# Optimization experiments

Measured on AMD Instinct MI355X. Metric: run time of the kernel, lower is better.

The kernel has to match this reference:

```python
import jax, jax.numpy as jnp
import numpy as np

H = 256          # encoder hidden per direction
D = 2 * H        # decoder hidden / bidirectional feature dim
IN = 2
OUT = 2
B = 64
T = 256
STEPS = 24       # hard-coded decoder loop length in the source


def gru_cell(x, h, Wih, Whh, bih, bhh):
    # PyTorch GRU cell: gate order (r, z, n)
    gi = x @ Wih.T + bih
    gh = h @ Whh.T + bhh
    ir, iz, inn = jnp.split(gi, 3, axis=-1)
    hr, hz, hn = jnp.split(gh, 3, axis=-1)
    r = jax.nn.sigmoid(ir + hr)
    z = jax.nn.sigmoid(iz + hz)
    n = jnp.tanh(inn + r * hn)
    return (1.0 - z) * n + z * h


def run_dir(xs, Wih, Whh, bih, bhh, reverse):
    # xs: (T, B, F) time-major; returns outputs (T, B, H) and last hidden (B, H)
    h0 = jnp.zeros((xs.shape[1], Whh.shape[-1]), xs.dtype)
    def step(h, xt):
        h2 = gru_cell(xt, h, Wih, Whh, bih, bhh)
        return h2, h2
    h_last, ys = jax.lax.scan(step, h0, xs, reverse=reverse)
    return ys, h_last


def setup_inputs():
    keys = jax.random.split(jax.random.key(0), 24)
    k = iter(keys)
    def rn(shape, s):
        return jax.random.normal(next(k), shape, jnp.float32) * s
    se = 1.0 / np.sqrt(H)
    sd = 1.0 / np.sqrt(D)
    return {
        "x": rn((B, T, IN), 1.0),
        "enc_Wih0": rn((2, 3 * H, IN), se),
        "enc_Whh0": rn((2, 3 * H, H), se),
        "enc_bih0": rn((2, 3 * H), se),
        "enc_bhh0": rn((2, 3 * H), se),
        "enc_Wih": rn((2, 2, 3 * H, D), se),
        "enc_Whh": rn((2, 2, 3 * H, H), se),
        "enc_bih": rn((2, 2, 3 * H), se),
        "enc_bhh": rn((2, 2, 3 * H), se),
        "dec_Wih": rn((3, 3 * D, D), sd),
        "dec_Whh": rn((3, 3 * D, D), sd),
        "dec_bih": rn((3, 3 * D), sd),
        "dec_bhh": rn((3, 3 * D), sd),
        "fc_con_W": rn((D, 2 * D), sd),
        "fc_con_b": rn((D,), sd),
        "attn_W": rn((D, 2 * D), sd),
        "attn_b": rn((D,), sd),
        "v": jax.random.uniform(next(k), (D,), jnp.float32),  # torch.rand init
        "fc_W": rn((OUT, D), sd),
        "fc_b": rn((OUT,), sd),
    }


def reference(x, enc_Wih0, enc_Whh0, enc_bih0, enc_bhh0,
              enc_Wih, enc_Whh, enc_bih, enc_bhh,
              dec_Wih, dec_Whh, dec_bih, dec_bhh,
              fc_con_W, fc_con_b, attn_W, attn_b, v, fc_W, fc_b):
    # ---- bidirectional 3-layer GRU encoder ----
    seq = x.transpose(1, 0, 2)  # (T, B, IN) time-major
    hf_list, hb_list = [], []
    for l in range(3):
        if l == 0:
            Wf, Uf, bf, cf = enc_Wih0[0], enc_Whh0[0], enc_bih0[0], enc_bhh0[0]
            Wb, Ub, bb, cb = enc_Wih0[1], enc_Whh0[1], enc_bih0[1], enc_bhh0[1]
        else:
            Wf, Uf, bf, cf = enc_Wih[l-1, 0], enc_Whh[l-1, 0], enc_bih[l-1, 0], enc_bhh[l-1, 0]
            Wb, Ub, bb, cb = enc_Wih[l-1, 1], enc_Whh[l-1, 1], enc_bih[l-1, 1], enc_bhh[l-1, 1]
        yf, hf = run_dir(seq, Wf, Uf, bf, cf, False)
        yb, hb = run_dir(seq, Wb, Ub, bb, cb, True)
        seq = jnp.concatenate([yf, yb], axis=-1)
        hf_list.append(hf)
        hb_list.append(hb)
    enc_out = seq.transpose(1, 0, 2)  # (B, T, D)
    # hidden_decoder = cat(forward, backward) per layer -> (3, B, D)
    hidden = jnp.stack([jnp.concatenate([f, b], axis=-1)
                        for f, b in zip(hf_list, hb_list)])
    dec_in = enc_out[:, -1, :]  # (B, D)

    # additive attention: energy = tanh(W [h; enc_out] + b); precompute enc part
    attn_Wh = attn_W[:, :D]
    attn_We = attn_W[:, D:]
    enc_proj = jnp.einsum('bte,de->btd', enc_out, attn_We)  # (B, T, D)

    def dec_step(carry, _):
        d_in, hid = carry
        hq = hid[-1] @ attn_Wh.T                               # (B, D)
        energy = jnp.tanh(hq[:, None, :] + enc_proj + attn_b)  # (B, T, D)
        scores = jnp.einsum('btd,d->bt', energy, v)
        aw = jax.nn.softmax(scores, axis=1)                    # (B, T)
        ctx = jnp.einsum('bt,btd->bd', aw, enc_out)            # (B, D)
        inp = jnp.concatenate([d_in, ctx], axis=-1) @ fc_con_W.T + fc_con_b
        new_h = []
        for l in range(3):  # 3-layer unidirectional decoder GRU, single step
            hl = gru_cell(inp, hid[l], dec_Wih[l], dec_Whh[l], dec_bih[l], dec_bhh[l])
            new_h.append(hl)
            inp = hl
        out_step = inp @ fc_W.T + fc_b
        return (inp, jnp.stack(new_h)), out_step

    _, outs = jax.lax.scan(dec_step, (dec_in, hidden), None, length=STEPS)
    return outs.transpose(1, 0, 2)  # (B, 24, OUT)
```

## Files before the change

### kernel.cpp

```cpp
#include <hip/hip_runtime.h>

typedef unsigned short u16;
typedef unsigned int u32;
typedef _Float16 f16;
typedef f16   f16x2 __attribute__((ext_vector_type(2)));
typedef f16   f16x8 __attribute__((ext_vector_type(8)));
typedef float f32x4 __attribute__((ext_vector_type(4)));

#define MFMA16(a,b,c) __builtin_amdgcn_mfma_f32_16x16x32_f16((a),(b),(c),0,0,0)

__device__ __forceinline__ float sigm_(float x){ return 1.f/(1.f + __expf(-x)); }
__device__ __forceinline__ float tanh_(float x){ return 1.f - 2.f/(1.f + __expf(2.f*x)); }
__device__ __forceinline__ float clampf(float x, float c){
  if (!(x > -c)) x = -c;
  if (x > c) x = c;
  return x;
}
__device__ __forceinline__ f16x8 cvt8f(const float* p){
  const float4 a = *(const float4*)p;
  const float4 b = *(const float4*)(p+4);
  f16x8 r;
  r[0]=(f16)a.x; r[1]=(f16)a.y; r[2]=(f16)a.z; r[3]=(f16)a.w;
  r[4]=(f16)b.x; r[5]=(f16)b.y; r[6]=(f16)b.z; r[7]=(f16)b.w;
  return r;
}

__global__ void k_diag(float* out, int mib){
  const int i = blockIdx.x*256 + threadIdx.x;
  if (i < 3072) out[i] = 1000.f * (float)mib;
}

__global__ void k_prep_dec(const float* dWhh, const float* attnW, const float* fccon,
                           const float* dWih, f16* R3)
{
  long idx = (long)blockIdx.x*256 + threadIdx.x;
  const float* src; int rs, colOff = 0, NKS; long dst, loc;
  if (idx < 294912L) {
    loc = idx; const int m = (int)(loc / 98304); loc %= 98304;
    src = dWhh + (long)m*786432; rs = 512; NKS = 16; dst = (long)m*786432;
  } else if (idx < 327680L) {
    loc = idx - 294912L; src = attnW; colOff = 512; rs = 1024; NKS = 16; dst = 2359296L;
  } else if (idx < 393216L) {
    loc = idx - 327680L; src = fccon; rs = 1024; NKS = 32; dst = 2621440L;
  } else if (idx < 688128L) {
    loc = idx - 393216L; const int m = (int)(loc / 98304); loc %= 98304;
    src = dWih + (long)m*786432; rs = 512; NKS = 16; dst = 3440640L + (long)m*786432;
  } else if (idx < 720896L) {
    loc = idx - 688128L; src = attnW; colOff = 0; rs = 1024; NKS = 16; dst = 5799936L;
  } else return;
  const int lane = (int)(loc & 63);
  const long frag = loc >> 6;
  const int ks = (int)(frag % NKS);
  const long nt = frag / NKS;
  const int n  = (int)(nt*16 + (lane & 15));
  const int k0 = ks*32 + ((lane >> 4) << 3);
  const float* sp = src + (long)n*rs + colOff + k0;
  f16* dp = R3 + dst + loc*8;
  #pragma unroll
  for (int j = 0; j < 8; ++j) dp[j] = (f16)sp[j];
}

__global__ void k_gi0s(const float* __restrict__ x, const float* __restrict__ W,
                       const float* __restrict__ bi, f16* __restrict__ gi,
                       int seg, int BH, int lbh, int b0)
{
  const long idx = (long)blockIdx.x*256 + threadIdx.x;
  const int v = (int)(idx % 24);
  long rest = idx / 24;
  const int tid = (int)(rest & 511); rest >>= 9;
  const int bq = (int)(rest & ((1 << (lbh-4)) - 1)); rest >>= (lbh-4);
  const int s = (int)(rest & 63);
  const int d = (int)(rest >> 6);
  const int r = v / 6, rem = v % 6, i = rem / 3, g = rem % 3;
  const int w = tid >> 6, q = (tid >> 4) & 3, lo = tid & 15;
  const int n = g*256 + (2*w + i)*16 + lo;
  const int b = bq*16 + q*4 + r;
  const int t = d ? (255 - (seg*64 + s)) : (seg*64 + s);
  const float x0 = x[(((b0+b)<<8) + t)*2];
  const float x1 = x[(((b0+b)<<8) + t)*2 + 1];
  const long wi = ((long)d*768 + n)*2;
  gi[idx] = (f16)clampf(x0*W[wi] + x1*W[wi+1] + bi[d*768 + n], 32.f);
}

#define GIE(G, vv) ((float)((vv) < 8 ? (G)[0][(vv)&7] : ((vv) < 16 ? (G)[1][(vv)-8] : (G)[2][(vv)-16])))

__global__ __launch_bounds__(512, 1) void k_enc_seg(
    const f16* __restrict__ gi, const float* __restrict__ Wraw,
    const float* __restrict__ bhh, f16* __restrict__ seq, int ostr,
    f16* __restrict__ fin, float* __restrict__ hcar, int seg, int BH)
{
  const int tid = threadIdx.x;
  const int w = tid >> 6, lane = tid & 63;
  const int lo16 = lane & 15, quad = lane >> 4;
  const int nbq = BH >> 4;
  const int dir = blockIdx.x / nbq, bq = blockIdx.x % nbq;

  __shared__ f16 h16[4][16][264];

  const float* mat = Wraw + (long)dir*196608;
  f16x8 wr[6][8];
  #pragma unroll
  for (int p = 0; p < 3; ++p)
    #pragma unroll
    for (int i = 0; i < 2; ++i) {
      const int n = (p*16 + 2*w + i)*16 + lo16;
      #pragma unroll
      for (int ks = 0; ks < 8; ++ks)
        wr[p*2+i][ks] = cvt8f(mat + (long)n*256 + ks*32 + quad*8);
    }
  float bh_[3][2];
  #pragma unroll
  for (int p = 0; p < 3; ++p)
    #pragma unroll
    for (int i = 0; i < 2; ++i)
      bh_[p][i] = bhh[dir*768 + p*256 + (2*w+i)*16 + lo16];

  float hreg[2][4];
  if (seg == 0) {
    #pragma unroll
    for (int i = 0; i < 2; ++i)
      #pragma unroll
      for (int r = 0; r < 4; ++r) {
        hreg[i][r] = 0.f;
        h16[0][quad*4 + r][(2*w+i)*16 + lo16] = (f16)0.f;
      }
  } else {
    #pragma unroll
    for (int i = 0; i < 2; ++i) {
      const int c = (2*w+i)*16 + lo16;
      #pragma unroll
      for (int r = 0; r < 4; ++r) {
        const float v = hcar[((dir*BH) + bq*16 + quad*4 + r)*256 + c];
        hreg[i][r] = v;
        h16[0][quad*4 + r][c] = (f16)v;
      }
    }
  }

  const long gstep = (long)nbq*512*24;
  const f16* gbase = gi + (((long)dir*64*nbq + bq)*512 + tid)*24;
  f16x8 g0[3], g1[3];
  { const f16x8* gp = (const f16x8*)gbase; g0[0]=gp[0]; g0[1]=gp[1]; g0[2]=gp[2]; }

  const int frow = tid >> 5;
  const int fcol = (tid & 31) * 8;

  for (int s = 0; s < 64; ++s) {
    __syncthreads();
    if (s >= 2) {
      const int so = s - 2;
      const int t2 = dir ? (255 - (seg*64 + so)) : (seg*64 + so);
      const f16x8 hv = *(const f16x8*)&h16[(so+1)&3][frow][fcol];
      *(f16x8*)&seq[((long)t2*ostr + bq*16 + frow)*512 + dir*256 + fcol] = hv;
    }
    f32x4 acc[6];
    #pragma unroll
    for (int q = 0; q < 6; ++q) acc[q] = (f32x4){0.f,0.f,0.f,0.f};
    #pragma unroll
    for (int ks = 0; ks < 8; ++ks) {
      const f16x8 a = *(const f16x8*)&h16[s&3][lo16][ks*32 + quad*8];
      #pragma unroll
      for (int q = 0; q < 6; ++q)
        acc[q] = MFMA16(a, wr[q][ks], acc[q]);
    }
    if (s < 63) {
      const f16x8* gp = (const f16x8*)(gbase + (long)(s+1)*gstep);
      g1[0]=gp[0]; g1[1]=gp[1]; g1[2]=gp[2];
    }
    #pragma unroll
    for (int i = 0; i < 2; ++i) {
      const int c = (2*w+i)*16 + lo16;
      #pragma unroll
      for (int r = 0; r < 4; ++r) {
        const int row = quad*4 + r;
        const int v = r*6 + i*3;
        const float gir = GIE(g0, v);
        const float giz = GIE(g0, v+1);
        const float gin = GIE(g0, v+2);
        const float rv = sigm_(gir + acc[i][r]   + bh_[0][i]);
        const float zv = sigm_(giz + acc[2+i][r] + bh_[1][i]);
        const float nv = tanh_(gin + rv*(acc[4+i][r] + bh_[2][i]));
        float hn = (1.f - zv)*nv + zv*hreg[i][r];
        hn = clampf(hn, 2.f);
        hreg[i][r] = hn;
        h16[(s+1)&3][row][c] = (f16)hn;
        if (seg == 3 && s == 63) fin[(bq*16 + row)*512 + dir*256 + c] = (f16)hn;
      }
    }
    g0[0]=g1[0]; g0[1]=g1[1]; g0[2]=g1[2];
  }
  __syncthreads();
  #pragma unroll
  for (int so = 62; so < 64; ++so) {
    const int t2 = dir ? (255 - (seg*64 + so)) : (seg*64 + so);
    const f16x8 hv = *(const f16x8*)&h16[(so+1)&3][frow][fcol];
    *(f16x8*)&seq[((long)t2*ostr + bq*16 + frow)*512 + dir*256 + fcol] = hv;
  }
  #pragma unroll
  for (int i = 0; i < 2; ++i) {
    const int c = (2*w+i)*16 + lo16;
    #pragma unroll
    for (int r = 0; r < 4; ++r)
      hcar[((dir*BH) + bq*16 + quad*4 + r)*256 + c] = hreg[i][r];
  }
}

__global__ void k_gemm(const f16* __restrict__ A, int K,
                       const f16* __restrict__ Bsw, const float* __restrict__ Braw,
                       long bzs, int ldb, int koff,
                       const float* __restrict__ bias, int biaszs,
                       void* __restrict__ Cv, long czs, int ldc, int mode,
                       int tb0, int tb1, int tdirsgn, int lbh, int abstr, float cv)
{
  const int tid = threadIdx.x, w = tid>>6, lane = tid&63;
  const int lo16 = lane&15, quad = lane>>4;
  const int m0 = blockIdx.x*64 + w*16;
  const int n0 = blockIdx.y*128;
  const int z  = blockIdx.z;
  const int tbase = z ? tb1 : tb0;
  const int tdir  = z ? -tdirsgn : tdirsgn;
  const int NKS = K >> 5;
  const int mrow = m0 + lo16;
  const long arow = (long)(tbase + tdir*(mrow >> lbh))*abstr + (mrow & ((1<<lbh)-1));
  const f16* Ap = A + arow*K + quad*8;
  f32x4 acc[8];
  #pragma unroll
  for (int i=0;i<8;++i) acc[i]=(f32x4){0.f,0.f,0.f,0.f};
  if (Bsw) {
    const f16* Bp = Bsw + (long)z*bzs;
    for (int ks = 0; ks < NKS; ++ks) {
      const f16x8 a = *(const f16x8*)(Ap + ks*32);
      #pragma unroll
      for (int nt = 0; nt < 8; ++nt) {
        const f16x8 b = *(const f16x8*)(Bp + (((long)((n0>>4)+nt)*NKS + ks) << 9) + lane*8);
        acc[nt] = MFMA16(a, b, acc[nt]);
      }
    }
  } else {
    const float* Bp = Braw + (long)z*bzs;
    for (int ks = 0; ks < NKS; ++ks) {
      const f16x8 a = *(const f16x8*)(Ap + ks*32);
      #pragma unroll
      for (int nt = 0; nt < 8; ++nt) {
        const f16x8 b = cvt8f(Bp + (long)(n0 + nt*16 + lo16)*ldb + koff + ks*32 + quad*8);
        acc[nt] = MFMA16(a, b, acc[nt]);
      }
    }
  }
  #pragma unroll
  for (int nt = 0; nt < 8; ++nt) {
    const int n = n0 + nt*16 + lo16;
    const float bv = bias ? bias[z*biaszs + n] : 0.f;
    #pragma unroll
    for (int r = 0; r < 4; ++r) {
      const int m = m0 + quad*4 + r;
      const float val = clampf(acc[nt][r] + bv, cv);
      if (mode == 2) {
        const int s_ = m >> lbh, b_ = m & ((1<<lbh)-1);
        const int bq_ = b_ >> 4, q_ = (b_ >> 2) & 3, r_ = b_ & 3;
        const int g_ = n >> 8, j_ = (n >> 4) & 15, lo_ = n & 15;
        const long idx = ((((long)z*64 + s_)*(1<<(lbh-4)) + bq_)*512
                          + ((j_>>1)*64 + q_*16 + lo_))*24 + r_*6 + (j_&1)*3 + g_;
        ((f16*)Cv)[idx] = (f16)val;
      } else if (mode == 1)
        ((f16*)Cv)[(long)z*czs + (long)m*ldc + n] = (f16)val;
      else
        ((float*)Cv)[(long)z*czs + (long)m*ldc + n] = val;
    }
  }
}

__global__ void k_score(const f16* __restrict__ seq, const f16* __restrict__ We,
                        const float* __restrict__ hq, const float* __restrict__ ab,
                        const float* __restrict__ vp, float* __restrict__ S)
{
  const int t = blockIdx.x, tid = threadIdx.x;
  const int w = tid>>6, lane = tid&63, lo16 = lane&15, quad = lane>>4;
  __shared__ float svab[1024];
  for (int i = tid; i < 512; i += 256) { svab[i] = vp[i]; svab[512+i] = ab[i]; }
  __syncthreads();
  f32x4 acc[32];
  #pragma unroll
  for (int i=0;i<32;++i) acc[i]=(f32x4){0.f,0.f,0.f,0.f};
  const f16* Ap = seq + ((long)t*64 + w*16 + lo16)*512 + quad*8;
  for (int ks = 0; ks < 16; ++ks) {
    const f16x8 a = *(const f16x8*)(Ap + ks*32);
    #pragma unroll
    for (int nt = 0; nt < 32; ++nt) {
      const f16x8 b = *(const f16x8*)(We + (((long)nt*16 + ks) << 9) + lane*8);
      acc[nt] = MFMA16(a, b, acc[nt]);
    }
  }
  #pragma unroll
  for (int r = 0; r < 4; ++r) {
    const int b = w*16 + quad*4 + r;
    float sc = 0.f;
    #pragma unroll
    for (int nt = 0; nt < 32; ++nt) {
      const int n = nt*16 + lo16;
      sc += svab[n] * tanh_(acc[nt][r] + hq[(b<<9) + n] + svab[512+n]);
    }
    sc += __shfl_xor(sc, 1, 64); sc += __shfl_xor(sc, 2, 64);
    sc += __shfl_xor(sc, 4, 64); sc += __shfl_xor(sc, 8, 64);
    if (lo16 == 0) S[(b<<8) + t] = clampf(sc, 256.f);
  }
}

__global__ void k_attnctx(const float* __restrict__ S, const f16* __restrict__ enc,
                          f16* __restrict__ cat)
{
  const int b = blockIdx.x, tid = threadIdx.x;
  __shared__ float ssc[256], srd[256];
  const float sc = clampf(S[(b<<8) + tid], 256.f);
  srd[tid] = sc; __syncthreads();
  for (int off = 128; off > 0; off >>= 1) { if (tid < off) srd[tid] = fmaxf(srd[tid], srd[tid+off]); __syncthreads(); }
  const float mx = srd[0]; __syncthreads();
  const float e = __expf(sc - mx);
  srd[tid] = e; __syncthreads();
  for (int off = 128; off > 0; off >>= 1) { if (tid < off) srd[tid] += srd[tid+off]; __syncthreads(); }
  const float inv = 1.f / srd[0]; __syncthreads();
  ssc[tid] = e * inv; __syncthreads();
  float c0 = 0.f, c1 = 0.f;
  for (int tt = 0; tt < 256; ++tt) {
    const float awt = ssc[tt];
    const f16* ep = enc + (((long)tt*64 + b) << 9);
    c0 += awt * (float)ep[tid];
    c1 += awt * (float)ep[256 + tid];
  }
  cat[(b<<10) + 512 + tid] = (f16)clampf(c0, 4.f);
  cat[(b<<10) + 768 + tid] = (f16)clampf(c1, 4.f);
}

__global__ void k_dec_init(const f16* __restrict__ fin, const f16* __restrict__ seq,
                           f16* __restrict__ hb16, float* __restrict__ hf32,
                           f16* __restrict__ cat)
{
  const int idx = blockIdx.x*256 + threadIdx.x;
  const int d = idx & 511, b = (idx >> 9) & 63, l = idx >> 15;
  if (l < 3) {
    const float v = clampf((float)fin[((long)l<<15) + (b<<9) + d], 2.f);
    hb16[(long)l*65536 + (b<<9) + d] = (f16)v;
    hf32[(long)l*32768 + (b<<9) + d] = v;
  } else {
    cat[(b<<10) + d] = seq[((long)255*64 + b)*512 + d];
  }
}

__global__ __launch_bounds__(512, 1) void k_attn(
    const f16* __restrict__ seq, const f16* __restrict__ ep,
    const float* __restrict__ hf2, const f16* __restrict__ cat,
    const f16* __restrict__ whsw, const f16* __restrict__ fcsw,
    const float* __restrict__ fcconB, const float* __restrict__ vp,
    f16* __restrict__ inp, const float* __restrict__ fcW,
    const float* __restrict__ fcb, float* __restrict__ out, int step)
{
  const int b = blockIdx.x;
  const int tid = threadIdx.x, w = tid >> 6, lane = tid & 63;
  const int quad = lane >> 4;
  __shared__ float hsm[512];
  __shared__ float cats[1024];
  __shared__ float hqs[512];
  __shared__ float aw[256];
  __shared__ float red[8*512];
  hsm[tid]  = hf2[(b<<9) + tid];
  cats[tid] = (float)cat[(b<<10) + tid];
  __syncthreads();
  if (w < 2 && step > 0) {
    float p = 0.f;
    #pragma unroll
    for (int j = 0; j < 8; ++j) p += fcW[(w<<9) + lane*8 + j] * hsm[lane*8 + j];
    p += __shfl_xor(p,1,64); p += __shfl_xor(p,2,64); p += __shfl_xor(p,4,64);
    p += __shfl_xor(p,8,64); p += __shfl_xor(p,16,64); p += __shfl_xor(p,32,64);
    if (lane == 0) out[(b*24 + step-1)*2 + w] = clampf(p + fcb[w], 128.f);
  }
  #pragma unroll
  for (int i = 0; i < 4; ++i) {
    const int nt = w*4 + i;
    float p = 0.f;
    for (int ks = 0; ks < 16; ++ks) {
      const f16x8 wv = *(const f16x8*)(whsw + (((long)nt*16 + ks)<<9) + lane*8);
      const float4 ha = *(const float4*)&hsm[ks*32 + quad*8];
      const float4 hb = *(const float4*)&hsm[ks*32 + quad*8 + 4];
      p += (float)wv[0]*ha.x + (float)wv[1]*ha.y + (float)wv[2]*ha.z + (float)wv[3]*ha.w
         + (float)wv[4]*hb.x + (float)wv[5]*hb.y + (float)wv[6]*hb.z + (float)wv[7]*hb.w;
    }
    p += __shfl_xor(p,16,64); p += __shfl_xor(p,32,64);
    if (lane < 16) hqs[nt*16 + lane] = p;
  }
  __syncthreads();
  float hq8[8], v8[8];
  #pragma unroll
  for (int j = 0; j < 8; ++j) { hq8[j] = hqs[lane*8+j]; v8[j] = vp[lane*8+j]; }
  #pragma unroll 2
  for (int i = 0; i < 32; ++i) {
    const int t = w*32 + i;
    const f16x8 e = *(const f16x8*)(ep + (((long)t*64 + b)<<9) + lane*8);
    float s = 0.f;
    #pragma unroll
    for (int j = 0; j < 8; ++j) s += v8[j]*tanh_((float)e[j] + hq8[j]);
    s += __shfl_xor(s,1,64); s += __shfl_xor(s,2,64); s += __shfl_xor(s,4,64);
    s += __shfl_xor(s,8,64); s += __shfl_xor(s,16,64); s += __shfl_xor(s,32,64);
    if (lane == 0) aw[t] = clampf(s, 256.f);
  }
  __syncthreads();
  if (tid < 64) {
    float s0=aw[tid], s1=aw[tid+64], s2=aw[tid+128], s3=aw[tid+192];
    float mx = fmaxf(fmaxf(s0,s1), fmaxf(s2,s3));
    mx = fmaxf(mx, __shfl_xor(mx,1,64)); mx = fmaxf(mx, __shfl_xor(mx,2,64));
    mx = fmaxf(mx, __shfl_xor(mx,4,64)); mx = fmaxf(mx, __shfl_xor(mx,8,64));
    mx = fmaxf(mx, __shfl_xor(mx,16,64)); mx = fmaxf(mx, __shfl_xor(mx,32,64));
    const float e0=__expf(s0-mx), e1=__expf(s1-mx), e2=__expf(s2-mx), e3=__expf(s3-mx);
    float sm = e0+e1+e2+e3;
    sm += __shfl_xor(sm,1,64); sm += __shfl_xor(sm,2,64); sm += __shfl_xor(sm,4,64);
    sm += __shfl_xor(sm,8,64); sm += __shfl_xor(sm,16,64); sm += __shfl_xor(sm,32,64);
    const float inv = 1.f/sm;
    aw[tid]=e0*inv; aw[tid+64]=e1*inv; aw[tid+128]=e2*inv; aw[tid+192]=e3*inv;
  }
  __syncthreads();
  float c8[8];
  #pragma unroll
  for (int j = 0; j < 8; ++j) c8[j] = 0.f;
  #pragma unroll 2
  for (int i = 0; i < 32; ++i) {
    const int t = w*32 + i;
    const f16x8 e = *(const f16x8*)(seq + (((long)t*64 + b)<<9) + lane*8);
    const float awt = aw[t];
    #pragma unroll
    for (int j = 0; j < 8; ++j) c8[j] += awt*(float)e[j];
  }
  #pragma unroll
  for (int j = 0; j < 8; ++j) red[(w<<9) + lane*8 + j] = c8[j];
  __syncthreads();
  {
    float s = 0.f;
    #pragma unroll
    for (int ww = 0; ww < 8; ++ww) s += red[(ww<<9) + tid];
    cats[512 + tid] = clampf(s, 4.f);
  }
  __syncthreads();
  #pragma unroll
  for (int i = 0; i < 4; ++i) {
    const int nt = w*4 + i;
    float p = 0.f;
    for (int ks = 0; ks < 32; ++ks) {
      const f16x8 wv = *(const f16x8*)(fcsw + (((long)nt*32 + ks)<<9) + lane*8);
      const float4 ca = *(const float4*)&cats[ks*32 + quad*8];
      const float4 cb = *(const float4*)&cats[ks*32 + quad*8 + 4];
      p += (float)wv[0]*ca.x + (float)wv[1]*ca.y + (float)wv[2]*ca.z + (float)wv[3]*ca.w
         + (float)wv[4]*cb.x + (float)wv[5]*cb.y + (float)wv[6]*cb.z + (float)wv[7]*cb.w;
    }
    p += __shfl_xor(p,16,64); p += __shfl_xor(p,32,64);
    if (lane < 16) inp[(b<<9) + nt*16 + lane] = (f16)clampf(p + fcconB[nt*16+lane], 64.f);
  }
}

__global__ void k_cell(const f16* __restrict__ inp, const f16* __restrict__ WihSw,
                       const f16* __restrict__ WhhSw, const float* __restrict__ bih,
                       const float* __restrict__ bhh, float* __restrict__ hf32,
                       const f16* __restrict__ hin, f16* __restrict__ hout,
                       f16* __restrict__ cat)
{
  const int tid = threadIdx.x, w = tid>>6, lane = tid&63;
  const int lo16 = lane&15, quad = lane>>4;
  const int Wt  = (blockIdx.x & 7)*4 + w;
  const int mi0 = (blockIdx.x >> 3)*2;
  f32x4 arz[4], an_[4];
  #pragma unroll
  for (int i=0;i<4;++i){ arz[i]=(f32x4){0.f,0.f,0.f,0.f}; an_[i]=(f32x4){0.f,0.f,0.f,0.f}; }
  #pragma unroll 2
  for (int kk = 0; kk < 16; ++kk) {
    const f16x8 b0 = *(const f16x8*)(WihSw + (((long)Wt*16 + kk)<<9)      + lane*8);
    const f16x8 b1 = *(const f16x8*)(WihSw + (((long)(32+Wt)*16 + kk)<<9) + lane*8);
    const f16x8 b2 = *(const f16x8*)(WihSw + (((long)(64+Wt)*16 + kk)<<9) + lane*8);
    #pragma unroll
    for (int m = 0; m < 2; ++m) {
      const f16x8 a = *(const f16x8*)&inp[(((mi0+m)*16 + lo16)<<9) + kk*32 + quad*8];
      arz[m]   = MFMA16(a, b0, arz[m]);
      arz[2+m] = MFMA16(a, b1, arz[2+m]);
      an_[m]   = MFMA16(a, b2, an_[m]);
    }
  }
  #pragma unroll 2
  for (int kk = 0; kk < 16; ++kk) {
    const f16x8 b0 = *(const f16x8*)(WhhSw + (((long)Wt*16 + kk)<<9)      + lane*8);
    const f16x8 b1 = *(const f16x8*)(WhhSw + (((long)(32+Wt)*16 + kk)<<9) + lane*8);
    const f16x8 b2 = *(const f16x8*)(WhhSw + (((long)(64+Wt)*16 + kk)<<9) + lane*8);
    #pragma unroll
    for (int m = 0; m < 2; ++m) {
      const f16x8 a = *(const f16x8*)&hin[(((mi0+m)*16 + lo16)<<9) + kk*32 + quad*8];
      arz[m]   = MFMA16(a, b0, arz[m]);
      arz[2+m] = MFMA16(a, b1, arz[2+m]);
      an_[2+m] = MFMA16(a, b2, an_[2+m]);
    }
  }
  const int c = Wt*16 + lo16;
  const float brz0 = bih[c]     + bhh[c];
  const float brz1 = bih[512+c] + bhh[512+c];
  const float bin_ = bih[1024+c];
  const float bhn_ = bhh[1024+c];
  #pragma unroll
  for (int m = 0; m < 2; ++m)
    #pragma unroll
    for (int r = 0; r < 4; ++r) {
      const int row = (mi0+m)*16 + quad*4 + r;
      const float rv = sigm_(clampf(arz[m][r],64.f)   + brz0);
      const float zv = sigm_(clampf(arz[2+m][r],64.f) + brz1);
      const float nv = tanh_(clampf(an_[m][r],64.f) + bin_ + rv*(clampf(an_[2+m][r],64.f) + bhn_));
      const float ho = hf32[(row<<9) + c];
      float hn2 = (1.f - zv)*nv + zv*ho;
      hn2 = clampf(hn2, 2.f);
      hf32[(row<<9) + c] = hn2;
      hout[(row<<9) + c] = (f16)hn2;
      if (cat) cat[(row<<10) + c] = (f16)hn2;
    }
}

__global__ void k_cell_raw(const f16* __restrict__ inp, const float* __restrict__ WihRaw,
                           const f16* __restrict__ WhhSw, const float* __restrict__ bih,
                           const float* __restrict__ bhh, float* __restrict__ hf32,
                           const f16* __restrict__ hin, f16* __restrict__ hout,
                           f16* __restrict__ cat)
{
  const int tid = threadIdx.x, w = tid>>6, lane = tid&63;
  const int lo16 = lane&15, quad = lane>>4;
  const int Wt = blockIdx.x*4 + w;
  f32x4 arz[8], an_[8];
  #pragma unroll
  for (int i=0;i<8;++i){ arz[i]=(f32x4){0.f,0.f,0.f,0.f}; an_[i]=(f32x4){0.f,0.f,0.f,0.f}; }
  const int nr = Wt*16 + lo16;
  const float* Rr = WihRaw + (long)nr*512        + quad*8;
  const float* Rz = WihRaw + (long)(512+nr)*512  + quad*8;
  const float* Rn = WihRaw + (long)(1024+nr)*512 + quad*8;
  #pragma unroll 2
  for (int kk = 0; kk < 16; ++kk) {
    const f16x8 b0 = cvt8f(Rr + kk*32);
    const f16x8 b1 = cvt8f(Rz + kk*32);
    const f16x8 b2 = cvt8f(Rn + kk*32);
    #pragma unroll
    for (int mi = 0; mi < 4; ++mi) {
      const f16x8 a = *(const f16x8*)&inp[((mi*16 + lo16)<<9) + kk*32 + quad*8];
      arz[mi]   = MFMA16(a, b0, arz[mi]);
      arz[4+mi] = MFMA16(a, b1, arz[4+mi]);
      an_[mi]   = MFMA16(a, b2, an_[mi]);
    }
  }
  #pragma unroll 2
  for (int kk = 0; kk < 16; ++kk) {
    const f16x8 b0 = *(const f16x8*)(WhhSw + (((long)Wt*16 + kk)<<9)      + lane*8);
    const f16x8 b1 = *(const f16x8*)(WhhSw + (((long)(32+Wt)*16 + kk)<<9) + lane*8);
    const f16x8 b2 = *(const f16x8*)(WhhSw + (((long)(64+Wt)*16 + kk)<<9) + lane*8);
    #pragma unroll
    for (int mi = 0; mi < 4; ++mi) {
      const f16x8 a = *(const f16x8*)&hin[((mi*16 + lo16)<<9) + kk*32 + quad*8];
      arz[mi]   = MFMA16(a, b0, arz[mi]);
      arz[4+mi] = MFMA16(a, b1, arz[4+mi]);
      an_[4+mi] = MFMA16(a, b2, an_[4+mi]);
    }
  }
  const int c = Wt*16 + lo16;
  const float brz0 = bih[c]     + bhh[c];
  const float brz1 = bih[512+c] + bhh[512+c];
  const float bin_ = bih[1024+c];
  const float bhn_ = bhh[1024+c];
  #pragma unroll
  for (int mi = 0; mi < 4; ++mi)
    #pragma unroll
    for (int r = 0; r < 4; ++r) {
      const int row = mi*16 + quad*4 + r;
      const float rv = sigm_(clampf(arz[mi][r],64.f)   + brz0);
      const float zv = sigm_(clampf(arz[4+mi][r],64.f) + brz1);
      const float nv = tanh_(clampf(an_[mi][r],64.f) + bin_ + rv*(clampf(an_[4+mi][r],64.f) + bhn_));
      const float ho = hf32[(row<<9) + c];
      float hn2 = (1.f - zv)*nv + zv*ho;
      hn2 = clampf(hn2, 2.f);
      hf32[(row<<9) + c] = hn2;
      hout[(row<<9) + c] = (f16)hn2;
      if (cat) cat[(row<<10) + c] = (f16)hn2;
    }
}

__global__ void k_out(const float* __restrict__ h2, const float* __restrict__ fcW,
                      const float* __restrict__ fcb, float* __restrict__ out, int step)
{
  const int b = blockIdx.x, t = threadIdx.x;
  __shared__ float r0[256], r1[256];
  const float ha = clampf(h2[(b<<9) + t], 2.f);
  const float hb = clampf(h2[(b<<9) + 256 + t], 2.f);
  r0[t] = ha*fcW[t]     + hb*fcW[256+t];
  r1[t] = ha*fcW[512+t] + hb*fcW[768+t];
  __syncthreads();
  for (int off = 128; off > 0; off >>= 1) {
    if (t < off) { r0[t] += r0[t+off]; r1[t] += r1[t+off]; }
    __syncthreads();
  }
  if (t == 0) {
    out[(b*24 + step)*2]     = clampf(r0[0] + fcb[0], 128.f);
    out[(b*24 + step)*2 + 1] = clampf(r1[0] + fcb[1], 128.f);
  }
}

extern "C" void kernel_launch(void* const* d_in, const int* in_sizes, int n_in,
                              void* d_out, int out_size, void* d_ws, size_t ws_size,
                              hipStream_t stream) {
  const float* X      = (const float*)d_in[0];
  const float* eWih0  = (const float*)d_in[1];
  const float* eWhh0  = (const float*)d_in[2];
  const float* ebih0  = (const float*)d_in[3];
  const float* ebhh0  = (const float*)d_in[4];
  const float* eWih   = (const float*)d_in[5];
  const float* eWhh   = (const float*)d_in[6];
  const float* ebih   = (const float*)d_in[7];
  const float* ebhh   = (const float*)d_in[8];
  const float* dWih   = (const float*)d_in[9];
  const float* dWhh   = (const float*)d_in[10];
  const float* dbih   = (const float*)d_in[11];
  const float* dbhh   = (const float*)d_in[12];
  const float* fcconW = (const float*)d_in[13];
  const float* fcconB = (const float*)d_in[14];
  const float* attnW  = (const float*)d_in[15];
  const float* attnB  = (const float*)d_in[16];
  const float* vW     = (const float*)d_in[17];
  const float* fcW    = (const float*)d_in[18];
  const float* fcB    = (const float*)d_in[19];
  float* OUT = (float*)d_out;

  const long need_big  = 47054848L;
  const long need_half = 32964608L;
  f16* H = (f16*)d_ws;
  f16 *SEQ = H, *L1OUT, *GIB, *R3, *FIN, *HB, *CAT, *INP;
  float *HC;
  int BH, lbh, nh, l1ostr, l1abstr; long gdir;

  if ((long)ws_size >= need_big) {
    BH = 64; lbh = 6; nh = 1; l1ostr = 64; l1abstr = 64;
    L1OUT = H + 8388608L;
    GIB   = H + 16777216L;
    HC    = (float*)(H + 23068672L);
    FIN   = H + 23134208L;
    HB    = H + 23232512L;
    CAT   = H + 23429120L;
    INP   = H + 23494656L;
    gdir  = 3145728L;
  } else if ((long)ws_size >= need_half) {
    BH = 32; lbh = 5; nh = 2; l1ostr = 32; l1abstr = 32;
    L1OUT = H + 8388608L;
    GIB   = H + 12582912L;
    HC    = (float*)(H + 16023552L);
    FIN   = H + 16089088L;
    HB    = H + 16187392L;
    CAT   = H + 16384000L;
    INP   = H + 16449536L;
    gdir  = 1572864L;
  } else {
    k_diag<<<12, 256, 0, stream>>>(OUT, (int)(ws_size >> 20));
    return;
  }
  R3 = GIB;
  float* ST = (float*)(GIB + 3145728L);
  float* HQ = ST;
  float* HF = ST + 32768;
  float* S  = ST + 131072;
  const int nblk = 2*(BH>>4);
  const int gi0grid = (2*64*BH*768)/256;

  for (int h = 0; h < nh; ++h) {
    const int b0 = h*BH;
    for (int seg = 0; seg < 4; ++seg) {
      k_gi0s<<<gi0grid, 256, 0, stream>>>(X, eWih0, ebih0, GIB, seg, BH, lbh, b0);
      k_enc_seg<<<nblk, 512, 0, stream>>>(GIB, eWhh0, ebhh0, SEQ + (long)b0*512, 64,
                                          FIN + (long)b0*512, HC, seg, BH);
    }
    for (int seg = 0; seg < 4; ++seg) {
      k_gemm<<<dim3(BH, 6, 2), 256, 0, stream>>>(SEQ + (long)b0*512, 512,
          (const f16*)nullptr, eWih, 393216L, 512, 0, ebih, 768,
          GIB, gdir, 768, 2, seg*64, 255 - seg*64, 1, lbh, 64, 32.f);
      k_enc_seg<<<nblk, 512, 0, stream>>>(GIB, eWhh, ebhh, L1OUT, l1ostr,
                                          FIN + 32768 + (long)b0*512, HC, seg, BH);
    }
    for (int seg = 0; seg < 4; ++seg) {
      k_gemm<<<dim3(BH, 6, 2), 256, 0, stream>>>(L1OUT, 512,
          (const f16*)nullptr, eWih + 2L*393216, 393216L, 512, 0, ebih + 1536, 768,
          GIB, gdir, 768, 2, seg*64, 255 - seg*64, 1, lbh, l1abstr, 32.f);
      k_enc_seg<<<nblk, 512, 0, stream>>>(GIB, eWhh + 2L*196608, ebhh + 1536,
                                          SEQ + (long)b0*512, 64,
                                          FIN + 65536 + (long)b0*512, HC, seg, BH);
    }
  }

  if (BH == 64) {
    f16* EP    = L1OUT;
    f16* WIHSW = GIB + 3440640L;
    f16* WHSW  = GIB + 5799936L;

    k_prep_dec<<<2816, 256, 0, stream>>>(dWhh, attnW, fcconW, dWih, R3);
    k_gemm<<<dim3(256, 4, 1), 256, 0, stream>>>(SEQ, 512,
        R3 + 2359296L, (const float*)nullptr, 0L, 0, 0, attnB, 0,
        EP, 0L, 512, 1, 0, 0, 1, 6, 64, 32.f);
    k_dec_init<<<512, 256, 0, stream>>>(FIN, SEQ, HB, HF, CAT);

    for (int s = 0; s < 24; ++s) {
      const int p = s & 1;
      k_attn<<<64, 512, 0, stream>>>(SEQ, EP, HF + 2*32768, CAT, WHSW, R3 + 2621440L,
          fcconB, vW, INP, fcW, fcB, OUT, s);
      for (int l = 0; l < 3; ++l) {
        const f16* inl = (l == 0) ? INP : (HB + (2*(l-1) + (1-p))*32768L);
        k_cell<<<16, 256, 0, stream>>>(inl,
                  WIHSW + (long)l*786432, R3 + (long)l*786432,
                  dbih + l*1536, dbhh + l*1536, HF + (long)l*32768,
                  HB + (2*l + p)*32768L, HB + (2*l + (1-p))*32768L,
                  (l == 2) ? CAT : (f16*)nullptr);
      }
    }
    k_out<<<64, 256, 0, stream>>>(HF + 2*32768, fcW, fcB, OUT, 23);
  } else {
    k_prep_dec<<<1536, 256, 0, stream>>>(dWhh, attnW, fcconW, dWih, R3);
    k_dec_init<<<512, 256, 0, stream>>>(FIN, SEQ, HB, HF, CAT);

    for (int s = 0; s < 24; ++s) {
      const int p = s & 1;
      const f16* h2in = HB + (4 + p)*32768L;
      k_gemm<<<dim3(1,4,1), 256, 0, stream>>>(h2in, 512,
          (const f16*)nullptr, attnW, 0L, 1024, 0, (const float*)nullptr, 0,
          HQ, 0L, 512, 0, 0, 0, 0, 6, 64, 64.f);
      k_score<<<256, 256, 0, stream>>>(SEQ, R3 + 2359296L, HQ, attnB, vW, S);
      k_attnctx<<<64, 256, 0, stream>>>(S, SEQ, CAT);
      k_gemm<<<dim3(1,4,1), 256, 0, stream>>>(CAT, 1024,
          R3 + 2621440L, (const float*)nullptr, 0L, 0, 0, fcconB, 0,
          INP, 0L, 512, 1, 0, 0, 0, 6, 64, 64.f);
      for (int l = 0; l < 3; ++l) {
        const f16* inp = (l == 0) ? INP : (HB + (2*(l-1) + (1-p))*32768L);
        k_cell_raw<<<8, 256, 0, stream>>>(inp,
                  dWih + (long)l*786432, R3 + (long)l*786432,
                  dbih + l*1536, dbhh + l*1536, HF + (long)l*32768,
                  HB + (2*l + p)*32768L, HB + (2*l + (1-p))*32768L,
                  (l == 2) ? CAT : (f16*)nullptr);
      }
      k_out<<<64, 256, 0, stream>>>(HF + 2*32768, fcW, fcB, OUT, s);
    }
  }
}
```

Baseline: 6.783 ms.

## Widen encoder blocks to 1024 threads and fuse decoder GRU layers with grid barrier

The encoder recurrent kernel now runs 16 waves per block, each owning one 16-column tile per gate instead of two. This halves per-wave MFMA and register work on the serial critical path, and the gi layout is changed to match in both the producer kernel and the GEMM. The three per-step decoder GRU cell launches are fused into one kernel that uses a global atomic barrier across its 16 blocks between layers, which removes launch overhead. In exchange, it relies on all 16 blocks being co-resident and on counters that are zeroed in the init kernel.

```diff
diff --git a/kernel.cpp b/kernel.cpp
--- a/kernel.cpp
+++ b/kernel.cpp
@@ -4,6 +4,7 @@
 typedef unsigned int u32;
 typedef _Float16 f16;
 typedef f16   f16x2 __attribute__((ext_vector_type(2)));
+typedef f16   f16x4 __attribute__((ext_vector_type(4)));
 typedef f16   f16x8 __attribute__((ext_vector_type(8)));
 typedef float f32x4 __attribute__((ext_vector_type(4)));
 
@@ -23,6 +24,17 @@
   r[0]=(f16)a.x; r[1]=(f16)a.y; r[2]=(f16)a.z; r[3]=(f16)a.w;
   r[4]=(f16)b.x; r[5]=(f16)b.y; r[6]=(f16)b.z; r[7]=(f16)b.w;
   return r;
+}
+
+__device__ __forceinline__ void gbar_(u32* c, u32 nb){
+  __syncthreads();
+  __threadfence();
+  if (threadIdx.x == 0) {
+    __hip_atomic_fetch_add(c, 1u, __ATOMIC_RELAXED, __HIP_MEMORY_SCOPE_AGENT);
+    while (__hip_atomic_load(c, __ATOMIC_RELAXED, __HIP_MEMORY_SCOPE_AGENT) < nb) {}
+  }
+  __syncthreads();
+  __threadfence();
 }
 
 __global__ void k_diag(float* out, int mib){
@@ -64,16 +76,19 @@
                        const float* __restrict__ bi, f16* __restrict__ gi,
                        int seg, int BH, int lbh, int b0)
 {
-  const long idx = (long)blockIdx.x*256 + threadIdx.x;
-  const int v = (int)(idx % 24);
-  long rest = idx / 24;
-  const int tid = (int)(rest & 511); rest >>= 9;
-  const int bq = (int)(rest & ((1 << (lbh-4)) - 1)); rest >>= (lbh-4);
-  const int s = (int)(rest & 63);
-  const int d = (int)(rest >> 6);
-  const int r = v / 6, rem = v % 6, i = rem / 3, g = rem % 3;
+  const u32 idx = blockIdx.x*256 + threadIdx.x;
+  const int e = idx & 3;
+  const int tid = (idx >> 2) & 1023;
+  u32 up = idx >> 12;
+  const int chunk = up % 3; up /= 3;
+  const int nbq = 1 << (lbh - 4);
+  const int bq = up & (nbq - 1); up >>= (lbh - 4);
+  const int s = up & 63;
+  const int d = up >> 6;
+  const int v = chunk*4 + e;
+  const int r = v/3, g = v%3;
   const int w = tid >> 6, q = (tid >> 4) & 3, lo = tid & 15;
-  const int n = g*256 + (2*w + i)*16 + lo;
+  const int n = g*256 + w*16 + lo;
   const int b = bq*16 + q*4 + r;
   const int t = d ? (255 - (seg*64 + s)) : (seg*64 + s);
   const float x0 = x[(((b0+b)<<8) + t)*2];
@@ -82,9 +97,9 @@
   gi[idx] = (f16)clampf(x0*W[wi] + x1*W[wi+1] + bi[d*768 + n], 32.f);
 }
 
-#define GIE(G, vv) ((float)((vv) < 8 ? (G)[0][(vv)&7] : ((vv) < 16 ? (G)[1][(vv)-8] : (G)[2][(vv)-16])))
-
-__global__ __launch_bounds__(512, 1) void k_enc_seg(
+#define GIE(G, vv) ((float)(G)[(vv)>>2][(vv)&3])
+
+__global__ __launch_bounds__(1024, 1) void k_enc_seg(
     const f16* __restrict__ gi, const float* __restrict__ Wraw,
     const float* __restrict__ bhh, f16* __restrict__ seq, int ostr,
     f16* __restrict__ fin, float* __restrict__ hcar, int seg, int BH)
@@ -94,115 +109,97 @@
   const int lo16 = lane & 15, quad = lane >> 4;
   const int nbq = BH >> 4;
   const int dir = blockIdx.x / nbq, bq = blockIdx.x % nbq;
+  const int c = w*16 + lo16;
 
   __shared__ f16 h16[4][16][264];
 
   const float* mat = Wraw + (long)dir*196608;
-  f16x8 wr[6][8];
+  f16x8 wr[3][8];
   #pragma unroll
   for (int p = 0; p < 3; ++p)
     #pragma unroll
-    for (int i = 0; i < 2; ++i) {
-      const int n = (p*16 + 2*w + i)*16 + lo16;
-      #pragma unroll
-      for (int ks = 0; ks < 8; ++ks)
-        wr[p*2+i][ks] = cvt8f(mat + (long)n*256 + ks*32 + quad*8);
-    }
-  float bh_[3][2];
-  #pragma unroll
-  for (int p = 0; p < 3; ++p)
-    #pragma unroll
-    for (int i = 0; i < 2; ++i)
-      bh_[p][i] = bhh[dir*768 + p*256 + (2*w+i)*16 + lo16];
-
-  float hreg[2][4];
+    for (int ks = 0; ks < 8; ++ks)
+      wr[p][ks] = cvt8f(mat + (long)(p*256 + c)*256 + ks*32 + quad*8);
+  float bh_[3];
+  #pragma unroll
+  for (int p = 0; p < 3; ++p) bh_[p] = bhh[dir*768 + p*256 + c];
+
+  float hreg[4];
   if (seg == 0) {
     #pragma unroll
-    for (int i = 0; i < 2; ++i)
-      #pragma unroll
-      for (int r = 0; r < 4; ++r) {
-        hreg[i][r] = 0.f;
-        h16[0][quad*4 + r][(2*w+i)*16 + lo16] = (f16)0.f;
-      }
+    for (int r = 0; r < 4; ++r) {
+      hreg[r] = 0.f;
+      h16[0][quad*4 + r][c] = (f16)0.f;
+    }
   } else {
     #pragma unroll
-    for (int i = 0; i < 2; ++i) {
-      const int c = (2*w+i)*16 + lo16;
-      #pragma unroll
-      for (int r = 0; r < 4; ++r) {
-        const float v = hcar[((dir*BH) + bq*16 + quad*4 + r)*256 + c];
-        hreg[i][r] = v;
-        h16[0][quad*4 + r][c] = (f16)v;
-      }
-    }
-  }
-
-  const long gstep = (long)nbq*512*24;
-  const f16* gbase = gi + (((long)dir*64*nbq + bq)*512 + tid)*24;
-  f16x8 g0[3], g1[3];
-  { const f16x8* gp = (const f16x8*)gbase; g0[0]=gp[0]; g0[1]=gp[1]; g0[2]=gp[2]; }
-
-  const int frow = tid >> 5;
-  const int fcol = (tid & 31) * 8;
+    for (int r = 0; r < 4; ++r) {
+      const float v = hcar[((dir*BH) + bq*16 + quad*4 + r)*256 + c];
+      hreg[r] = v;
+      h16[0][quad*4 + r][c] = (f16)v;
+    }
+  }
+
+  const long gstep = (long)nbq*12288;
+  const f16* gp0 = gi + ((long)dir*64*nbq + bq)*12288 + tid*4;
+  f16x4 g0[3], g1[3];
+  g0[0] = *(const f16x4*)(gp0);
+  g0[1] = *(const f16x4*)(gp0 + 4096);
+  g0[2] = *(const f16x4*)(gp0 + 8192);
+
+  const int frow = tid >> 6;
+  const int fcol = lane*4;
+  const int t20 = dir ? (255 - seg*64) : (seg*64);
+  f16* fp = seq + ((long)t20*ostr + bq*16 + frow)*512 + dir*256 + fcol;
+  const long sadv = (dir ? -(long)ostr : (long)ostr)*512;
 
   for (int s = 0; s < 64; ++s) {
-    __syncthreads();
+    asm volatile("s_waitcnt lgkmcnt(0)\n\ts_barrier" ::: "memory");
     if (s >= 2) {
-      const int so = s - 2;
-      const int t2 = dir ? (255 - (seg*64 + so)) : (seg*64 + so);
-      const f16x8 hv = *(const f16x8*)&h16[(so+1)&3][frow][fcol];
-      *(f16x8*)&seq[((long)t2*ostr + bq*16 + frow)*512 + dir*256 + fcol] = hv;
-    }
-    f32x4 acc[6];
-    #pragma unroll
-    for (int q = 0; q < 6; ++q) acc[q] = (f32x4){0.f,0.f,0.f,0.f};
+      const f16x4 hv = *(const f16x4*)&h16[(s-1)&3][frow][fcol];
+      *(f16x4*)fp = hv;
+      fp += sadv;
+    }
+    f32x4 acc[3];
+    #pragma unroll
+    for (int p = 0; p < 3; ++p) acc[p] = (f32x4){0.f,0.f,0.f,0.f};
     #pragma unroll
     for (int ks = 0; ks < 8; ++ks) {
       const f16x8 a = *(const f16x8*)&h16[s&3][lo16][ks*32 + quad*8];
-      #pragma unroll
-      for (int q = 0; q < 6; ++q)
-        acc[q] = MFMA16(a, wr[q][ks], acc[q]);
+      acc[0] = MFMA16(a, wr[0][ks], acc[0]);
+      acc[1] = MFMA16(a, wr[1][ks], acc[1]);
+      acc[2] = MFMA16(a, wr[2][ks], acc[2]);
     }
     if (s < 63) {
-      const f16x8* gp = (const f16x8*)(gbase + (long)(s+1)*gstep);
-      g1[0]=gp[0]; g1[1]=gp[1]; g1[2]=gp[2];
-    }
-    #pragma unroll
-    for (int i = 0; i < 2; ++i) {
-      const int c = (2*w+i)*16 + lo16;
-      #pragma unroll
-      for (int r = 0; r < 4; ++r) {
-        const int row = quad*4 + r;
-        const int v = r*6 + i*3;
-        const float gir = GIE(g0, v);
-        const float giz = GIE(g0, v+1);
-        const float gin = GIE(g0, v+2);
-        const float rv = sigm_(gir + acc[i][r]   + bh_[0][i]);
-        const float zv = sigm_(giz + acc[2+i][r] + bh_[1][i]);
-        const float nv = tanh_(gin + rv*(acc[4+i][r] + bh_[2][i]));
-        float hn = (1.f - zv)*nv + zv*hreg[i][r];
-        hn = clampf(hn, 2.f);
-        hreg[i][r] = hn;
-        h16[(s+1)&3][row][c] = (f16)hn;
-        if (seg == 3 && s == 63) fin[(bq*16 + row)*512 + dir*256 + c] = (f16)hn;
-      }
+      const f16* gp = gp0 + (long)(s+1)*gstep;
+      g1[0] = *(const f16x4*)(gp);
+      g1[1] = *(const f16x4*)(gp + 4096);
+      g1[2] = *(const f16x4*)(gp + 8192);
+    }
+    #pragma unroll
+    for (int r = 0; r < 4; ++r) {
+      const int v = r*3;
+      const float rv = sigm_(GIE(g0, v)   + acc[0][r] + bh_[0]);
+      const float zv = sigm_(GIE(g0, v+1) + acc[1][r] + bh_[1]);
+      const float nv = tanh_(GIE(g0, v+2) + rv*(acc[2][r] + bh_[2]));
+      float hn = (1.f - zv)*nv + zv*hreg[r];
+      hn = clampf(hn, 2.f);
+      hreg[r] = hn;
+      h16[(s+1)&3][quad*4 + r][c] = (f16)hn;
+      if (seg == 3 && s == 63) fin[(bq*16 + quad*4 + r)*512 + dir*256 + c] = (f16)hn;
     }
     g0[0]=g1[0]; g0[1]=g1[1]; g0[2]=g1[2];
   }
   __syncthreads();
   #pragma unroll
   for (int so = 62; so < 64; ++so) {
-    const int t2 = dir ? (255 - (seg*64 + so)) : (seg*64 + so);
-    const f16x8 hv = *(const f16x8*)&h16[(so+1)&3][frow][fcol];
-    *(f16x8*)&seq[((long)t2*ostr + bq*16 + frow)*512 + dir*256 + fcol] = hv;
-  }
-  #pragma unroll
-  for (int i = 0; i < 2; ++i) {
-    const int c = (2*w+i)*16 + lo16;
-    #pragma unroll
-    for (int r = 0; r < 4; ++r)
-      hcar[((dir*BH) + bq*16 + quad*4 + r)*256 + c] = hreg[i][r];
-  }
+    const f16x4 hv = *(const f16x4*)&h16[(so+1)&3][frow][fcol];
+    *(f16x4*)fp = hv;
+    fp += sadv;
+  }
+  #pragma unroll
+  for (int r = 0; r < 4; ++r)
+    hcar[((dir*BH) + bq*16 + quad*4 + r)*256 + c] = hreg[r];
 }
 
 __global__ void k_gemm(const f16* __restrict__ A, int K,
@@ -257,10 +254,12 @@
       const float val = clampf(acc[nt][r] + bv, cv);
       if (mode == 2) {
         const int s_ = m >> lbh, b_ = m & ((1<<lbh)-1);
+        const int nbq_ = 1 << (lbh - 4);
         const int bq_ = b_ >> 4, q_ = (b_ >> 2) & 3, r_ = b_ & 3;
-        const int g_ = n >> 8, j_ = (n >> 4) & 15, lo_ = n & 15;
-        const long idx = ((((long)z*64 + s_)*(1<<(lbh-4)) + bq_)*512
-                          + ((j_>>1)*64 + q_*16 + lo_))*24 + r_*6 + (j_&1)*3 + g_;
+        const int g_ = n >> 8, c_ = n & 255;
+        const int tid_ = (c_ >> 4)*64 + q_*16 + (c_ & 15);
+        const int v_ = r_*3 + g_;
+        const long idx = (((long)(z*64 + s_)*nbq_ + bq_)*3 + (v_>>2))*4096 + tid_*4 + (v_&3);
         ((f16*)Cv)[idx] = (f16)val;
       } else if (mode == 1)
         ((f16*)Cv)[(long)z*czs + (long)m*ldc + n] = (f16)val;
@@ -333,9 +332,10 @@
 
 __global__ void k_dec_init(const f16* __restrict__ fin, const f16* __restrict__ seq,
                            f16* __restrict__ hb16, float* __restrict__ hf32,
-                           f16* __restrict__ cat)
+                           f16* __restrict__ cat, u32* __restrict__ cnt)
 {
   const int idx = blockIdx.x*256 + threadIdx.x;
+  if (idx < 64) cnt[idx] = 0;
   const int d = idx & 511, b = (idx >> 9) & 63, l = idx >> 15;
   if (l < 3) {
     const float v = clampf((float)fin[((long)l<<15) + (b<<9) + d], 2.f);
@@ -454,65 +454,77 @@
   }
 }
 
-__global__ void k_cell(const f16* __restrict__ inp, const f16* __restrict__ WihSw,
-                       const f16* __restrict__ WhhSw, const float* __restrict__ bih,
-                       const float* __restrict__ bhh, float* __restrict__ hf32,
-                       const f16* __restrict__ hin, f16* __restrict__ hout,
-                       f16* __restrict__ cat)
+__global__ void k_cell3(const f16* __restrict__ inp0, const f16* __restrict__ WihSw,
+                        const f16* __restrict__ WhhSw, const float* __restrict__ bihA,
+                        const float* __restrict__ bhhA, float* __restrict__ hfA,
+                        f16* __restrict__ hb, f16* __restrict__ cat, int p, u32* cnt)
 {
   const int tid = threadIdx.x, w = tid>>6, lane = tid&63;
   const int lo16 = lane&15, quad = lane>>4;
-  const int Wt  = (blockIdx.x & 7)*4 + w;
-  const int mi0 = (blockIdx.x >> 3)*2;
-  f32x4 arz[4], an_[4];
-  #pragma unroll
-  for (int i=0;i<4;++i){ arz[i]=(f32x4){0.f,0.f,0.f,0.f}; an_[i]=(f32x4){0.f,0.f,0.f,0.f}; }
-  #pragma unroll 2
-  for (int kk = 0; kk < 16; ++kk) {
-    const f16x8 b0 = *(const f16x8*)(WihSw + (((long)Wt*16 + kk)<<9)      + lane*8);
-    const f16x8 b1 = *(const f16x8*)(WihSw + (((long)(32+Wt)*16 + kk)<<9) + lane*8);
-    const f16x8 b2 = *(const f16x8*)(WihSw + (((long)(64+Wt)*16 + kk)<<9) + lane*8);
-    #pragma unroll
-    for (int m = 0; m < 2; ++m) {
-      const f16x8 a = *(const f16x8*)&inp[(((mi0+m)*16 + lo16)<<9) + kk*32 + quad*8];
-      arz[m]   = MFMA16(a, b0, arz[m]);
-      arz[2+m] = MFMA16(a, b1, arz[2+m]);
-      an_[m]   = MFMA16(a, b2, an_[m]);
-    }
-  }
-  #pragma unroll 2
-  for (int kk = 0; kk < 16; ++kk) {
-    const f16x8 b0 = *(const f16x8*)(WhhSw + (((long)Wt*16 + kk)<<9)      + lane*8);
-    const f16x8 b1 = *(const f16x8*)(WhhSw + (((long)(32+Wt)*16 + kk)<<9) + lane*8);
-    const f16x8 b2 = *(const f16x8*)(WhhSw + (((long)(64+Wt)*16 + kk)<<9) + lane*8);
-    #pragma unroll
-    for (int m = 0; m < 2; ++m) {
-      const f16x8 a = *(const f16x8*)&hin[(((mi0+m)*16 + lo16)<<9) + kk*32 + quad*8];
-      arz[m]   = MFMA16(a, b0, arz[m]);
-      arz[2+m] = MFMA16(a, b1, arz[2+m]);
-      an_[2+m] = MFMA16(a, b2, an_[2+m]);
-    }
-  }
-  const int c = Wt*16 + lo16;
-  const float brz0 = bih[c]     + bhh[c];
-  const float brz1 = bih[512+c] + bhh[512+c];
-  const float bin_ = bih[1024+c];
-  const float bhn_ = bhh[1024+c];
-  #pragma unroll
-  for (int m = 0; m < 2; ++m)
-    #pragma unroll
-    for (int r = 0; r < 4; ++r) {
-      const int row = (mi0+m)*16 + quad*4 + r;
-      const float rv = sigm_(clampf(arz[m][r],64.f)   + brz0);
-      const float zv = sigm_(clampf(arz[2+m][r],64.f) + brz1);
-      const float nv = tanh_(clampf(an_[m][r],64.f) + bin_ + rv*(clampf(an_[2+m][r],64.f) + bhn_));
-      const float ho = hf32[(row<<9) + c];
-      float hn2 = (1.f - zv)*nv + zv*ho;
-      hn2 = clampf(hn2, 2.f);
-      hf32[(row<<9) + c] = hn2;
-      hout[(row<<9) + c] = (f16)hn2;
-      if (cat) cat[(row<<10) + c] = (f16)hn2;
-    }
+  const int Wt  = ((int)blockIdx.x & 7)*4 + w;
+  const int mi0 = ((int)blockIdx.x >> 3)*2;
+  for (int l = 0; l < 3; ++l) {
+    const f16* inp = (l == 0) ? inp0 : (hb + (long)(2*(l-1) + (1-p))*32768);
+    const f16* WihL = WihSw + (long)l*786432;
+    const f16* WhhL = WhhSw + (long)l*786432;
+    const float* bih = bihA + l*1536;
+    const float* bhh = bhhA + l*1536;
+    float* hf32 = hfA + (long)l*32768;
+    const f16* hin = hb + (long)(2*l + p)*32768;
+    f16* hout = hb + (long)(2*l + (1-p))*32768;
+    f16* catp = (l == 2) ? cat : (f16*)nullptr;
+
+    f32x4 arz[4], an_[4];
+    #pragma unroll
+    for (int i=0;i<4;++i){ arz[i]=(f32x4){0.f,0.f,0.f,0.f}; an_[i]=(f32x4){0.f,0.f,0.f,0.f}; }
+    #pragma unroll 2
+    for (int kk = 0; kk < 16; ++kk) {
+      const f16x8 b0 = *(const f16x8*)(WihL + (((long)Wt*16 + kk)<<9)      + lane*8);
+      const f16x8 b1 = *(const f16x8*)(WihL + (((long)(32+Wt)*16 + kk)<<9) + lane*8);
+      const f16x8 b2 = *(const f16x8*)(WihL + (((long)(64+Wt)*16 + kk)<<9) + lane*8);
+      #pragma unroll
+      for (int m = 0; m < 2; ++m) {
+        const f16x8 a = *(const f16x8*)&inp[(((mi0+m)*16 + lo16)<<9) + kk*32 + quad*8];
+        arz[m]   = MFMA16(a, b0, arz[m]);
+        arz[2+m] = MFMA16(a, b1, arz[2+m]);
+        an_[m]   = MFMA16(a, b2, an_[m]);
+      }
+    }
+    #pragma unroll 2
+    for (int kk = 0; kk < 16; ++kk) {
+      const f16x8 b0 = *(const f16x8*)(WhhL + (((long)Wt*16 + kk)<<9)      + lane*8);
+      const f16x8 b1 = *(const f16x8*)(WhhL + (((long)(32+Wt)*16 + kk)<<9) + lane*8);
+      const f16x8 b2 = *(const f16x8*)(WhhL + (((long)(64+Wt)*16 + kk)<<9) + lane*8);
+      #pragma unroll
+      for (int m = 0; m < 2; ++m) {
+        const f16x8 a = *(const f16x8*)&hin[(((mi0+m)*16 + lo16)<<9) + kk*32 + quad*8];
+        arz[m]   = MFMA16(a, b0, arz[m]);
+        arz[2+m] = MFMA16(a, b1, arz[2+m]);
+        an_[2+m] = MFMA16(a, b2, an_[2+m]);
+      }
+    }
+    const int c = Wt*16 + lo16;
+    const float brz0 = bih[c]     + bhh[c];
+    const float brz1 = bih[512+c] + bhh[512+c];
+    const float bin_ = bih[1024+c];
+    const float bhn_ = bhh[1024+c];
+    #pragma unroll
+    for (int m = 0; m < 2; ++m)
+      #pragma unroll
+      for (int r = 0; r < 4; ++r) {
+        const int row = (mi0+m)*16 + quad*4 + r;
+        const float rv = sigm_(clampf(arz[m][r],64.f)   + brz0);
+        const float zv = sigm_(clampf(arz[2+m][r],64.f) + brz1);
+        const float nv = tanh_(clampf(an_[m][r],64.f) + bin_ + rv*(clampf(an_[2+m][r],64.f) + bhn_));
+        const float ho = hf32[(row<<9) + c];
+        float hn2 = (1.f - zv)*nv + zv*ho;
+        hn2 = clampf(hn2, 2.f);
+        hf32[(row<<9) + c] = hn2;
+        hout[(row<<9) + c] = (f16)hn2;
+        if (catp) catp[(row<<10) + c] = (f16)hn2;
+      }
+    if (l < 2) gbar_(cnt + l, 16);
+  }
 }
 
 __global__ void k_cell_raw(const f16* __restrict__ inp, const float* __restrict__ WihRaw,
@@ -660,6 +672,7 @@
   float* HQ = ST;
   float* HF = ST + 32768;
   float* S  = ST + 131072;
+  u32* CNT = (u32*)ST;
   const int nblk = 2*(BH>>4);
   const int gi0grid = (2*64*BH*768)/256;
 
@@ -667,21 +680,21 @@
     const int b0 = h*BH;
     for (int seg = 0; seg < 4; ++seg) {
       k_gi0s<<<gi0grid, 256, 0, stream>>>(X, eWih0, ebih0, GIB, seg, BH, lbh, b0);
-      k_enc_seg<<<nblk, 512, 0, stream>>>(GIB, eWhh0, ebhh0, SEQ + (long)b0*512, 64,
+      k_enc_seg<<<nblk, 1024, 0, stream>>>(GIB, eWhh0, ebhh0, SEQ + (long)b0*512, 64,
                                           FIN + (long)b0*512, HC, seg, BH);
     }
     for (int seg = 0; seg < 4; ++seg) {
       k_gemm<<<dim3(BH, 6, 2), 256, 0, stream>>>(SEQ + (long)b0*512, 512,
           (const f16*)nullptr, eWih, 393216L, 512, 0, ebih, 768,
           GIB, gdir, 768, 2, seg*64, 255 - seg*64, 1, lbh, 64, 32.f);
-      k_enc_seg<<<nblk, 512, 0, stream>>>(GIB, eWhh, ebhh, L1OUT, l1ostr,
+      k_enc_seg<<<nblk, 1024, 0, stream>>>(GIB, eWhh, ebhh, L1OUT, l1ostr,
                                           FIN + 32768 + (long)b0*512, HC, seg, BH);
     }
     for (int seg = 0; seg < 4; ++seg) {
       k_gemm<<<dim3(BH, 6, 2), 256, 0, stream>>>(L1OUT, 512,
           (const f16*)nullptr, eWih + 2L*393216, 393216L, 512, 0, ebih + 1536, 768,
           GIB, gdir, 768, 2, seg*64, 255 - seg*64, 1, lbh, l1abstr, 32.f);
-      k_enc_seg<<<nblk, 512, 0, stream>>>(GIB, eWhh + 2L*196608, ebhh + 1536,
+      k_enc_seg<<<nblk, 1024, 0, stream>>>(GIB, eWhh + 2L*196608, ebhh + 1536,
                                           SEQ + (long)b0*512, 64,
                                           FIN + 65536 + (long)b0*512, HC, seg, BH);
     }
@@ -696,25 +709,19 @@
     k_gemm<<<dim3(256, 4, 1), 256, 0, stream>>>(SEQ, 512,
         R3 + 2359296L, (const float*)nullptr, 0L, 0, 0, attnB, 0,
         EP, 0L, 512, 1, 0, 0, 1, 6, 64, 32.f);
-    k_dec_init<<<512, 256, 0, stream>>>(FIN, SEQ, HB, HF, CAT);
+    k_dec_init<<<512, 256, 0, stream>>>(FIN, SEQ, HB, HF, CAT, CNT);
 
     for (int s = 0; s < 24; ++s) {
       const int p = s & 1;
       k_attn<<<64, 512, 0, stream>>>(SEQ, EP, HF + 2*32768, CAT, WHSW, R3 + 2621440L,
           fcconB, vW, INP, fcW, fcB, OUT, s);
-      for (int l = 0; l < 3; ++l) {
-        const f16* inl = (l == 0) ? INP : (HB + (2*(l-1) + (1-p))*32768L);
-        k_cell<<<16, 256, 0, stream>>>(inl,
-                  WIHSW + (long)l*786432, R3 + (long)l*786432,
-                  dbih + l*1536, dbhh + l*1536, HF + (long)l*32768,
-                  HB + (2*l + p)*32768L, HB + (2*l + (1-p))*32768L,
-                  (l == 2) ? CAT : (f16*)nullptr);
-      }
+      k_cell3<<<16, 256, 0, stream>>>(INP, WIHSW, R3, dbih, dbhh, HF, HB, CAT,
+          p, CNT + s*2);
     }
     k_out<<<64, 256, 0, stream>>>(HF + 2*32768, fcW, fcB, OUT, 23);
   } else {
     k_prep_dec<<<1536, 256, 0, stream>>>(dWhh, attnW, fcconW, dWih, R3);
-    k_dec_init<<<512, 256, 0, stream>>>(FIN, SEQ, HB, HF, CAT);
+    k_dec_init<<<512, 256, 0, stream>>>(FIN, SEQ, HB, HF, CAT, (u32*)(S + 16000));
 
     for (int s = 0; s < 24; ++s) {
       const int p = s & 1;
```

After: 7.390 ms. 1.09x slower.
